# Kernel tuning notes

Measured on AMD Instinct MI355X. Metric: run time of the kernel, lower is better.

## Reference

```python
import itertools
import jax, jax.numpy as jnp
import numpy as np
from jax import lax

INT_STEPS = 7
DOWN = 2


def _sample(vol, coords):
    """Trilinear sample vol [C, D, H, W] at voxel coords [3, D2, H2, W2].
    Matches torch grid_sample(align_corners=True, padding_mode='zeros') after
    voxelmorph's voxel->[-1,1] normalization (i.e. plain voxel coordinates)."""
    dims = vol.shape[1:]
    c0f = jnp.floor(coords)
    frac = coords - c0f
    c0 = c0f.astype(jnp.int32)
    out = jnp.zeros((vol.shape[0],) + coords.shape[1:], vol.dtype)
    for corner in itertools.product((0, 1), repeat=3):
        w = jnp.ones(coords.shape[1:], vol.dtype)
        valid = True
        idxs = []
        for ax in range(3):
            idx = c0[ax] + corner[ax]
            w = w * (frac[ax] if corner[ax] else 1.0 - frac[ax])
            valid = valid & (idx >= 0) & (idx < dims[ax])
            idxs.append(jnp.clip(idx, 0, dims[ax] - 1))
        out = out + vol[:, idxs[0], idxs[1], idxs[2]] * (w * valid)
    return out


def _grid(shape, dtype):
    return jnp.stack(jnp.meshgrid(*[jnp.arange(s, dtype=dtype) for s in shape], indexing='ij'))


def _warp(src, flow):
    # SpatialTransformer: sample src at identity grid + flow (voxel coords)
    return _sample(src, _grid(src.shape[1:], flow.dtype) + flow)


def _resize(x, out_shape):
    # F.interpolate trilinear, align_corners=True: src = i*(in-1)/(out-1)
    coords = jnp.stack(jnp.meshgrid(
        *[jnp.linspace(0.0, s_in - 1.0, s_out, dtype=x.dtype)
          for s_in, s_out in zip(x.shape[1:], out_shape)], indexing='ij'))
    return _sample(x, coords)


def _flow_single(pos_flow, label):
    # pos_flow: [3, D, H, W], label: [1, D, H, W]
    full = pos_flow.shape[1:]
    down_shape = tuple(s // DOWN for s in full)
    # ResizeTransform(int_downsize): factor=1/DOWN<1 -> resize then scale
    f = _resize(pos_flow, down_shape) * (1.0 / DOWN)
    # VecInt: scaling and squaring
    f = f * (1.0 / (2 ** INT_STEPS))
    for _ in range(INT_STEPS):
        f = f + _warp(f, f)
    # ResizeTransform(1/int_downsize): factor=DOWN>1 -> scale then resize
    f = _resize(f * float(DOWN), full)
    moved = _warp(label, f)
    return moved, f


def setup_inputs() -> dict:
    key = jax.random.key(0)
    k1, k2, k3 = jax.random.split(key, 3)
    B, F, D, H, W = 1, 16, 128, 128, 128
    features = jax.random.normal(k1, (B, F, D, H, W), jnp.float32)
    moving_label = jax.random.uniform(k2, (B, 1, D, H, W), jnp.float32)
    # conv weight initialized Normal(0, 1e-5), bias zeros (as in module)
    weight = jax.random.normal(k3, (3, F, 3, 3, 3), jnp.float32) * 1e-5
    bias = jnp.zeros((3,), jnp.float32)
    return {"features": features, "moving_label": moving_label,
            "weight": weight, "bias": bias}


def reference(features, moving_label, weight, bias):
    pos_flow = lax.conv_general_dilated(
        features, weight, window_strides=(1, 1, 1),
        padding=[(1, 1)] * 3,
        dimension_numbers=('NCDHW', 'OIDHW', 'NCDHW'))
    pos_flow = pos_flow + bias[None, :, None, None, None]
    moved, flow = jax.vmap(_flow_single)(pos_flow, moving_label)
    return moved, flow
```

## Files before the change

kernel.cpp:

```cpp
#include <hip/hip_runtime.h>
#include <hip/hip_bf16.h>


#define V128 2097152
#define V64  262144

template <int C>
__device__ __forceinline__ void trisample(const float* __restrict__ vol,
                                          int D, int H, int W, int cstride,
                                          float cz, float cy, float cx,
                                          float* out) {
    float fz = floorf(cz), fy = floorf(cy), fx = floorf(cx);
    int iz = (int)fz, iy = (int)fy, ix = (int)fx;
    float tz = cz - fz, ty = cy - fy, tx = cx - fx;
#pragma unroll
    for (int c = 0; c < C; ++c) out[c] = 0.0f;
#pragma unroll
    for (int dz = 0; dz < 2; ++dz) {
#pragma unroll
        for (int dy = 0; dy < 2; ++dy) {
#pragma unroll
            for (int dx = 0; dx < 2; ++dx) {
                int z = iz + dz, y = iy + dy, x = ix + dx;
                float w = (dz ? tz : 1.0f - tz) *
                          (dy ? ty : 1.0f - ty) *
                          (dx ? tx : 1.0f - tx);
                bool valid = (z >= 0) && (z < D) && (y >= 0) && (y < H) &&
                             (x >= 0) && (x < W);
                int zc = min(max(z, 0), D - 1);
                int yc = min(max(y, 0), H - 1);
                int xc = min(max(x, 0), W - 1);
                int base = (zc * H + yc) * W + xc;
                float wv = valid ? w : 0.0f;
#pragma unroll
                for (int c = 0; c < C; ++c)
                    out[c] += vol[c * cstride + base] * wv;
            }
        }
    }
}

template <int SI>
__device__ __forceinline__ void lds_lerp3(const float* __restrict__ f,
                                          float pz, float py, float px,
                                          float* out) {
    constexpr int NI = SI * SI * SI;
    float fz = floorf(pz), fy = floorf(py), fx = floorf(px);
    int iz = (int)fz, iy = (int)fy, ix = (int)fx;
    float tz = pz - fz, ty = py - fy, tx = px - fx;
    int b = (iz * SI + iy) * SI + ix;
    float wz0 = 1.0f - tz, wy0 = 1.0f - ty, wx0 = 1.0f - tx;
#pragma unroll
    for (int c = 0; c < 3; ++c) {
        const float* fc = f + c * NI;
        float v00 = fc[b] * wx0 + fc[b + 1] * tx;
        float v01 = fc[b + SI] * wx0 + fc[b + SI + 1] * tx;
        float v10 = fc[b + SI * SI] * wx0 + fc[b + SI * SI + 1] * tx;
        float v11 = fc[b + SI * SI + SI] * wx0 + fc[b + SI * SI + SI + 1] * tx;
        out[c] = wz0 * (wy0 * v00 + ty * v01) + tz * (wy0 * v10 + ty * v11);
    }
}

template <int SI>
__device__ __forceinline__ void step_lds(const float* __restrict__ in,
                                         float* __restrict__ out, int tid) {
    constexpr int SO = SI - 2;
    constexpr int NI = SI * SI * SI;
    constexpr int NO = SO * SO * SO;
    for (int i = tid; i < NO; i += 256) {
        int xx = i % SO, yy = (i / SO) % SO, zz = i / (SO * SO);
        int la = ((zz + 1) * SI + (yy + 1)) * SI + (xx + 1);
        float fz = in[la], fy = in[la + NI], fx = in[la + 2 * NI];
        float sm[3];
        lds_lerp3<SI>(in, (zz + 1) + fz, (yy + 1) + fy, (xx + 1) + fx, sm);
        out[i] = fz + sm[0];
        out[i + NO] = fy + sm[1];
        out[i + 2 * NO] = fx + sm[2];
    }
}

__device__ __forceinline__ void step_to_global(const float* __restrict__ in,
                                               float* __restrict__ gout,
                                               int tx, int ty, int tz,
                                               int tid) {
    constexpr int SI = 10;
    constexpr int NI = SI * SI * SI;
    for (int i = tid; i < 512; i += 256) {
        int xx = i & 7, yy = (i >> 3) & 7, zz = i >> 6;
        int la = ((zz + 1) * SI + (yy + 1)) * SI + (xx + 1);
        float fz = in[la], fy = in[la + NI], fx = in[la + 2 * NI];
        float sm[3];
        lds_lerp3<SI>(in, (zz + 1) + fz, (yy + 1) + fy, (xx + 1) + fx, sm);
        int n = ((tz + zz) << 12) + ((ty + yy) << 6) + (tx + xx);
        gout[n] = fz + sm[0];
        gout[n + V64] = fy + sm[1];
        gout[n + 2 * V64] = fx + sm[2];
    }
}

__global__ __launch_bounds__(256) void conv_kernel(
    const float* __restrict__ feat, const float* __restrict__ weight,
    const float* __restrict__ bias, float* __restrict__ pos_flow) {
    __shared__ float smem[2][3960];
    const int tid = threadIdx.x;
    const int x0 = blockIdx.x * 64, y0 = blockIdx.y * 4, z0 = blockIdx.z * 8;
    const int lx = tid & 63, ly = tid >> 6;

    int goff[16];
    unsigned vmask = 0;
    {
        int xx = tid % 66;
        int r = tid / 66;
        int yy = r % 6;
        int zz = r / 6;
#pragma unroll
        for (int k = 0; k < 16; ++k) {
            bool intile = (k < 15) || (tid < 120);
            int gx = x0 + xx - 1, gy = y0 + yy - 1, gz = z0 + zz - 1;
            bool ok = intile && ((unsigned)gx < 128u) &&
                      ((unsigned)gy < 128u) && ((unsigned)gz < 128u);
            goff[k] = (gz << 14) + (gy << 7) + gx;
            if (ok) vmask |= (1u << k);
            xx += 58;
            yy += 3;
            if (xx >= 66) { xx -= 66; yy += 1; }
            if (yy >= 6) { yy -= 6; zz += 1; }
        }
    }

    typedef __attribute__((ext_vector_type(2))) float f32x2;
    f32x2 acc[3][4];
#pragma unroll
    for (int o = 0; o < 3; ++o)
#pragma unroll
        for (int zp = 0; zp < 4; ++zp) acc[o][zp] = (f32x2)(0.0f);

    {
        float vals[16];
#pragma unroll
        for (int k = 0; k < 16; ++k) {
            vals[k] = 0.0f;
            if (vmask & (1u << k)) vals[k] = feat[goff[k]];
        }
#pragma unroll
        for (int k = 0; k < 16; ++k)
            if (k < 15 || tid < 120) smem[0][tid + 256 * k] = vals[k];
    }

    for (int c = 0; c < 16; ++c) {
        __syncthreads();
        if (c + 1 < 16) {
            const float* fc = feat + ((c + 1) << 21);
            float* buf = smem[(c + 1) & 1];
            float vals[16];
#pragma unroll
            for (int k = 0; k < 16; ++k) {
                vals[k] = 0.0f;
                if (vmask & (1u << k)) vals[k] = fc[goff[k]];
            }
#pragma unroll
            for (int k = 0; k < 16; ++k)
                if (k < 15 || tid < 120) buf[tid + 256 * k] = vals[k];
        }
        const float* buf = smem[c & 1];
        const float* wc = weight + c * 27;
#pragma unroll
        for (int dy = 0; dy < 3; ++dy) {
#pragma unroll
            for (int dx = 0; dx < 3; ++dx) {
                const float* p = buf + (ly + dy) * 66 + lx + dx;
                float v[10];
#pragma unroll
                for (int zz = 0; zz < 10; ++zz) v[zz] = p[zz * 396];
#pragma unroll
                for (int dz = 0; dz < 3; ++dz) {
#pragma unroll
                    for (int o = 0; o < 3; ++o) {
                        float w = wc[o * 432 + dz * 9 + dy * 3 + dx];
#pragma unroll
                        for (int zp = 0; zp < 4; ++zp) {
                            acc[o][zp].x += v[2 * zp + dz] * w;
                            acc[o][zp].y += v[2 * zp + dz + 1] * w;
                        }
                    }
                }
            }
        }
    }

#pragma unroll
    for (int o = 0; o < 3; ++o) {
        float b = bias[o];
#pragma unroll
        for (int zp = 0; zp < 4; ++zp) {
            int z = z0 + 2 * zp;
            int base = o * V128 + ((y0 + ly) << 7) + x0 + lx;
            pos_flow[base + (z << 14)] = acc[o][zp].x + b;
            pos_flow[base + ((z + 1) << 14)] = acc[o][zp].y + b;
        }
    }
}

__global__ __launch_bounds__(256) void f2_kernel(
    const float* __restrict__ pos_flow, float* __restrict__ gout) {
    __shared__ float A[3 * 2744];
    __shared__ float B[3 * 1728];
    const int tid = threadIdx.x;
    const int tx = blockIdx.x * 8, ty = blockIdx.y * 8, tz = blockIdx.z * 8;
    const int rbx = tx - 3, rby = ty - 3, rbz = tz - 3;
    const float s2 = 127.0f / 63.0f;
    const float k = 1.0f / 256.0f;
    for (int i = tid; i < 2744; i += 256) {
        int xx = i % 14, yy = (i / 14) % 14, zz = i / 196;
        int gz = rbz + zz, gy = rby + yy, gx = rbx + xx;
        float v[3] = {0.0f, 0.0f, 0.0f};
        if ((unsigned)gz < 64u && (unsigned)gy < 64u && (unsigned)gx < 64u)
            trisample<3>(pos_flow, 128, 128, 128, V128, gz * s2, gy * s2,
                         gx * s2, v);
        A[i] = v[0] * k;
        A[i + 2744] = v[1] * k;
        A[i + 2 * 2744] = v[2] * k;
    }
    __syncthreads();
    step_lds<14>(A, B, tid);
    __syncthreads();
    step_lds<12>(B, A, tid);
    __syncthreads();
    step_to_global(A, gout, tx, ty, tz, tid);
}

__global__ __launch_bounds__(256) void f3_kernel(
    const float* __restrict__ gin, float* __restrict__ gout) {
    __shared__ float A[3 * 2744];
    __shared__ float B[3 * 1728];
    const int tid = threadIdx.x;
    const int tx = blockIdx.x * 8, ty = blockIdx.y * 8, tz = blockIdx.z * 8;
    const int rbx = tx - 3, rby = ty - 3, rbz = tz - 3;
    for (int i = tid; i < 2744; i += 256) {
        int xx = i % 14, yy = (i / 14) % 14, zz = i / 196;
        int gz = rbz + zz, gy = rby + yy, gx = rbx + xx;
        float v0 = 0.0f, v1 = 0.0f, v2 = 0.0f;
        if ((unsigned)gz < 64u && (unsigned)gy < 64u && (unsigned)gx < 64u) {
            int n = (gz << 12) + (gy << 6) + gx;
            v0 = gin[n];
            v1 = gin[n + V64];
            v2 = gin[n + 2 * V64];
        }
        A[i] = v0;
        A[i + 2744] = v1;
        A[i + 2 * 2744] = v2;
    }
    __syncthreads();
    step_lds<14>(A, B, tid);
    __syncthreads();
    step_lds<12>(B, A, tid);
    __syncthreads();
    step_to_global(A, gout, tx, ty, tz, tid);
}

__global__ __launch_bounds__(256) void f4_kernel(
    const float* __restrict__ gin, const float* __restrict__ label,
    float* __restrict__ moved, float* __restrict__ flow) {
    __shared__ float A[3 * 2197];
    __shared__ float B[3 * 1331];
    const int tid = threadIdx.x;
    const int ttx = blockIdx.x, tty = blockIdx.y, ttz = blockIdx.z;
    const int r0x = (1008 * ttx) / 127 - 1;
    const int r0y = (1008 * tty) / 127 - 1;
    const int r0z = (1008 * ttz) / 127 - 1;
    const int rbx = r0x - 1, rby = r0y - 1, rbz = r0z - 1;
    for (int i = tid; i < 2197; i += 256) {
        int xx = i % 13, yy = (i / 13) % 13, zz = i / 169;
        int gz = rbz + zz, gy = rby + yy, gx = rbx + xx;
        float v0 = 0.0f, v1 = 0.0f, v2 = 0.0f;
        if ((unsigned)gz < 64u && (unsigned)gy < 64u && (unsigned)gx < 64u) {
            int n = (gz << 12) + (gy << 6) + gx;
            v0 = gin[n];
            v1 = gin[n + V64];
            v2 = gin[n + 2 * V64];
        }
        A[i] = v0;
        A[i + 2197] = v1;
        A[i + 2 * 2197] = v2;
    }
    __syncthreads();
    step_lds<13>(A, B, tid);
    __syncthreads();
    const float s3 = 63.0f / 127.0f;
    for (int i = tid; i < 4096; i += 256) {
        int lx = i & 15, ly = (i >> 4) & 15, lz = i >> 8;
        int gx = ttx * 16 + lx, gy = tty * 16 + ly, gz = ttz * 16 + lz;
        float f[3];
        lds_lerp3<11>(B, gz * s3 - (float)r0z, gy * s3 - (float)r0y,
                      gx * s3 - (float)r0x, f);
        float fz = 2.0f * f[0], fy = 2.0f * f[1], fx = 2.0f * f[2];
        int m = (gz << 14) + (gy << 7) + gx;
        flow[m] = fz;
        flow[m + V128] = fy;
        flow[m + 2 * V128] = fx;
        float mv[1];
        trisample<1>(label, 128, 128, 128, 0, gz + fz, gy + fy, gx + fx, mv);
        moved[m] = mv[0];
    }
}

extern "C" void kernel_launch(void* const* d_in, const int* in_sizes, int n_in,
                              void* d_out, int out_size, void* d_ws,
                              size_t ws_size, hipStream_t stream) {
    const float* features = (const float*)d_in[0];
    const float* label = (const float*)d_in[1];
    const float* weight = (const float*)d_in[2];
    const float* bias = (const float*)d_in[3];
    float* out = (float*)d_out;
    float* moved = out;
    float* flow = out + V128;
    float* fA = (float*)d_ws;
    float* fB = fA + 3 * V64;

    conv_kernel<<<dim3(2, 32, 16), 256, 0, stream>>>(features, weight, bias,
                                                     flow);
    f2_kernel<<<dim3(8, 8, 8), 256, 0, stream>>>(flow, fA);
    f3_kernel<<<dim3(8, 8, 8), 256, 0, stream>>>(fA, fB);
    f4_kernel<<<dim3(8, 8, 8), 256, 0, stream>>>(fB, label, moved, flow);
}
```

Baseline: 329.0 us.

## Rewrite 3D conv in packed fp16 FMA with z-pair LDS layout

Moves the conv's multiply-accumulate from fp32 to packed half2 FMAs. Weights are pre-packed and scaled by 1024 in a small extra kernel, and features are staged into LDS as fp16 pairs along z, with shifted pairs built by bit operations. Tiles become 32x4x8 with 128 threads, and the packed weights are written into the output buffer as scratch. This halves FMA instruction count and LDS footprint, but accumulating in fp16 loses precision and may break tolerance.

After: 394.9 us. 20.0% more time.

```diff
diff --git a/kernel.cpp b/kernel.cpp
--- a/kernel.cpp
+++ b/kernel.cpp
@@ -1,9 +1,12 @@
 #include <hip/hip_runtime.h>
 #include <hip/hip_bf16.h>
+#include <hip/hip_fp16.h>
 
 
 #define V128 2097152
 #define V64  262144
+
+typedef __fp16 __attribute__((ext_vector_type(2))) half2_raw;
 
 template <int C>
 __device__ __forceinline__ void trisample(const float* __restrict__ vol,
@@ -36,6 +39,147 @@
                 for (int c = 0; c < C; ++c)
                     out[c] += vol[c * cstride + base] * wv;
             }
+        }
+    }
+}
+
+__global__ __launch_bounds__(256) void pack_weights(
+    const float* __restrict__ w, unsigned* __restrict__ wpk) {
+    int i = blockIdx.x * 256 + threadIdx.x;
+    if (i < 1296) {
+        int c = i / 81, r = i % 81;
+        int t = r / 9, rr = r % 9;
+        int o = rr / 3, dz = rr % 3;
+        int dy = t / 3, dx = t % 3;
+        float wv = w[(o * 16 + c) * 27 + dz * 9 + dy * 3 + dx] * 1024.0f;
+        half2_raw p = __builtin_amdgcn_cvt_pkrtz(wv, wv);
+        wpk[i] = __builtin_bit_cast(unsigned, p);
+    }
+}
+
+__global__ __launch_bounds__(128) void conv_kernel(
+    const float* __restrict__ feat, const unsigned* __restrict__ wpk,
+    const float* __restrict__ bias, float* __restrict__ pos_flow) {
+    __shared__ unsigned smem[2][1020];
+    const int tid = threadIdx.x;
+    const int x0 = blockIdx.x * 32, y0 = blockIdx.y * 4, z0 = blockIdx.z * 8;
+    const int lx = tid & 31, ly = tid >> 5;
+
+    int coloff[2];
+    bool cval[2];
+#pragma unroll
+    for (int s = 0; s < 2; ++s) {
+        int cc = tid + 128 * s;
+        cval[s] = false;
+        coloff[s] = 0;
+        if (cc < 204) {
+            int xx = cc % 34, yy = cc / 34;
+            int gx = x0 + xx - 1, gy = y0 + yy - 1;
+            cval[s] = ((unsigned)gx < 128u) && ((unsigned)gy < 128u);
+            coloff[s] = (min(max(gy, 0), 127) << 7) + min(max(gx, 0), 127);
+        }
+    }
+
+    __half2 acc2[3][4];
+#pragma unroll
+    for (int o = 0; o < 3; ++o)
+#pragma unroll
+        for (int p = 0; p < 4; ++p)
+            acc2[o][p] = __builtin_bit_cast(__half2, 0u);
+
+    auto stage = [&](int ch, unsigned* buf) {
+        const float* fc = feat + (ch << 21);
+#pragma unroll
+        for (int s = 0; s < 2; ++s) {
+            int cc = tid + 128 * s;
+            if (cc < 204) {
+                float v[10];
+#pragma unroll
+                for (int k = 0; k < 10; ++k) {
+                    int gz = z0 - 1 + k;
+                    int gzc = min(max(gz, 0), 127);
+                    float t = fc[(gzc << 14) + coloff[s]];
+                    v[k] = (cval[s] && ((unsigned)gz < 128u)) ? t : 0.0f;
+                }
+#pragma unroll
+                for (int j = 0; j < 5; ++j) {
+                    half2_raw p =
+                        __builtin_amdgcn_cvt_pkrtz(v[2 * j], v[2 * j + 1]);
+                    buf[cc * 5 + j] = __builtin_bit_cast(unsigned, p);
+                }
+            }
+        }
+    };
+
+    stage(0, smem[0]);
+
+    for (int c = 0; c < 16; ++c) {
+        __syncthreads();
+        if (c + 1 < 16) stage(c + 1, smem[(c + 1) & 1]);
+        const unsigned* buf = smem[c & 1];
+        const unsigned* wc = wpk + c * 81;
+#pragma unroll
+        for (int dy = 0; dy < 3; ++dy) {
+#pragma unroll
+            for (int dx = 0; dx < 3; ++dx) {
+                int cc = (ly + dy) * 34 + (lx + dx);
+                unsigned h0 = buf[cc * 5 + 0];
+                unsigned h1 = buf[cc * 5 + 1];
+                unsigned h2 = buf[cc * 5 + 2];
+                unsigned h3 = buf[cc * 5 + 3];
+                unsigned h4 = buf[cc * 5 + 4];
+                unsigned s0 = (h1 << 16) | (h0 >> 16);
+                unsigned s1 = (h2 << 16) | (h1 >> 16);
+                unsigned s2 = (h3 << 16) | (h2 >> 16);
+                unsigned s3 = (h4 << 16) | (h3 >> 16);
+                const int tb = (dy * 3 + dx) * 9;
+#pragma unroll
+                for (int o = 0; o < 3; ++o) {
+                    __half2 w0 = __builtin_bit_cast(__half2, wc[tb + o * 3]);
+                    __half2 w1 =
+                        __builtin_bit_cast(__half2, wc[tb + o * 3 + 1]);
+                    __half2 w2 =
+                        __builtin_bit_cast(__half2, wc[tb + o * 3 + 2]);
+                    acc2[o][0] = __hfma2(__builtin_bit_cast(__half2, h0), w0,
+                                         acc2[o][0]);
+                    acc2[o][1] = __hfma2(__builtin_bit_cast(__half2, h1), w0,
+                                         acc2[o][1]);
+                    acc2[o][2] = __hfma2(__builtin_bit_cast(__half2, h2), w0,
+                                         acc2[o][2]);
+                    acc2[o][3] = __hfma2(__builtin_bit_cast(__half2, h3), w0,
+                                         acc2[o][3]);
+                    acc2[o][0] = __hfma2(__builtin_bit_cast(__half2, s0), w1,
+                                         acc2[o][0]);
+                    acc2[o][1] = __hfma2(__builtin_bit_cast(__half2, s1), w1,
+                                         acc2[o][1]);
+                    acc2[o][2] = __hfma2(__builtin_bit_cast(__half2, s2), w1,
+                                         acc2[o][2]);
+                    acc2[o][3] = __hfma2(__builtin_bit_cast(__half2, s3), w1,
+                                         acc2[o][3]);
+                    acc2[o][0] = __hfma2(__builtin_bit_cast(__half2, h1), w2,
+                                         acc2[o][0]);
+                    acc2[o][1] = __hfma2(__builtin_bit_cast(__half2, h2), w2,
+                                         acc2[o][1]);
+                    acc2[o][2] = __hfma2(__builtin_bit_cast(__half2, h3), w2,
+                                         acc2[o][2]);
+                    acc2[o][3] = __hfma2(__builtin_bit_cast(__half2, h4), w2,
+                                         acc2[o][3]);
+                }
+            }
+        }
+    }
+
+    const float ds = 1.0f / 1024.0f;
+#pragma unroll
+    for (int o = 0; o < 3; ++o) {
+        float b = bias[o];
+        int base = o * V128 + ((y0 + ly) << 7) + x0 + lx;
+#pragma unroll
+        for (int p = 0; p < 4; ++p) {
+            int z = z0 + 2 * p;
+            pos_flow[base + (z << 14)] = __low2float(acc2[o][p]) * ds + b;
+            pos_flow[base + ((z + 1) << 14)] =
+                __high2float(acc2[o][p]) * ds + b;
         }
     }
 }
@@ -95,109 +239,6 @@
         gout[n] = fz + sm[0];
         gout[n + V64] = fy + sm[1];
         gout[n + 2 * V64] = fx + sm[2];
-    }
-}
-
-__global__ __launch_bounds__(256) void conv_kernel(
-    const float* __restrict__ feat, const float* __restrict__ weight,
-    const float* __restrict__ bias, float* __restrict__ pos_flow) {
-    __shared__ float smem[2][3960];
-    const int tid = threadIdx.x;
-    const int x0 = blockIdx.x * 64, y0 = blockIdx.y * 4, z0 = blockIdx.z * 8;
-    const int lx = tid & 63, ly = tid >> 6;
-
-    int goff[16];
-    unsigned vmask = 0;
-    {
-        int xx = tid % 66;
-        int r = tid / 66;
-        int yy = r % 6;
-        int zz = r / 6;
-#pragma unroll
-        for (int k = 0; k < 16; ++k) {
-            bool intile = (k < 15) || (tid < 120);
-            int gx = x0 + xx - 1, gy = y0 + yy - 1, gz = z0 + zz - 1;
-            bool ok = intile && ((unsigned)gx < 128u) &&
-                      ((unsigned)gy < 128u) && ((unsigned)gz < 128u);
-            goff[k] = (gz << 14) + (gy << 7) + gx;
-            if (ok) vmask |= (1u << k);
-            xx += 58;
-            yy += 3;
-            if (xx >= 66) { xx -= 66; yy += 1; }
-            if (yy >= 6) { yy -= 6; zz += 1; }
-        }
-    }
-
-    typedef __attribute__((ext_vector_type(2))) float f32x2;
-    f32x2 acc[3][4];
-#pragma unroll
-    for (int o = 0; o < 3; ++o)
-#pragma unroll
-        for (int zp = 0; zp < 4; ++zp) acc[o][zp] = (f32x2)(0.0f);
-
-    {
-        float vals[16];
-#pragma unroll
-        for (int k = 0; k < 16; ++k) {
-            vals[k] = 0.0f;
-            if (vmask & (1u << k)) vals[k] = feat[goff[k]];
-        }
-#pragma unroll
-        for (int k = 0; k < 16; ++k)
-            if (k < 15 || tid < 120) smem[0][tid + 256 * k] = vals[k];
-    }
-
-    for (int c = 0; c < 16; ++c) {
-        __syncthreads();
-        if (c + 1 < 16) {
-            const float* fc = feat + ((c + 1) << 21);
-            float* buf = smem[(c + 1) & 1];
-            float vals[16];
-#pragma unroll
-            for (int k = 0; k < 16; ++k) {
-                vals[k] = 0.0f;
-                if (vmask & (1u << k)) vals[k] = fc[goff[k]];
-            }
-#pragma unroll
-            for (int k = 0; k < 16; ++k)
-                if (k < 15 || tid < 120) buf[tid + 256 * k] = vals[k];
-        }
-        const float* buf = smem[c & 1];
-        const float* wc = weight + c * 27;
-#pragma unroll
-        for (int dy = 0; dy < 3; ++dy) {
-#pragma unroll
-            for (int dx = 0; dx < 3; ++dx) {
-                const float* p = buf + (ly + dy) * 66 + lx + dx;
-                float v[10];
-#pragma unroll
-                for (int zz = 0; zz < 10; ++zz) v[zz] = p[zz * 396];
-#pragma unroll
-                for (int dz = 0; dz < 3; ++dz) {
-#pragma unroll
-                    for (int o = 0; o < 3; ++o) {
-                        float w = wc[o * 432 + dz * 9 + dy * 3 + dx];
-#pragma unroll
-                        for (int zp = 0; zp < 4; ++zp) {
-                            acc[o][zp].x += v[2 * zp + dz] * w;
-                            acc[o][zp].y += v[2 * zp + dz + 1] * w;
-                        }
-                    }
-                }
-            }
-        }
-    }
-
-#pragma unroll
-    for (int o = 0; o < 3; ++o) {
-        float b = bias[o];
-#pragma unroll
-        for (int zp = 0; zp < 4; ++zp) {
-            int z = z0 + 2 * zp;
-            int base = o * V128 + ((y0 + ly) << 7) + x0 + lx;
-            pos_flow[base + (z << 14)] = acc[o][zp].x + b;
-            pos_flow[base + ((z + 1) << 14)] = acc[o][zp].y + b;
-        }
     }
 }
 
@@ -316,8 +357,10 @@
     float* flow = out + V128;
     float* fA = (float*)d_ws;
     float* fB = fA + 3 * V64;
-
-    conv_kernel<<<dim3(2, 32, 16), 256, 0, stream>>>(features, weight, bias,
+    unsigned* wpk = (unsigned*)moved;
+
+    pack_weights<<<6, 256, 0, stream>>>(weight, wpk);
+    conv_kernel<<<dim3(4, 32, 16), 128, 0, stream>>>(features, wpk, bias,
                                                      flow);
     f2_kernel<<<dim3(8, 8, 8), 256, 0, stream>>>(flow, fA);
     f3_kernel<<<dim3(8, 8, 8), 256, 0, stream>>>(fA, fB);
```
